# Optimization experiments

Hardware: AMD Instinct MI355X
Metric: run time of the kernel (lower is better)

The kernel has to match this reference:

```python
import jax, jax.numpy as jnp
import numpy as np

N = 50000      # nodes
E = 800000     # directed edges (before self-loops)
IN = 100       # ogbn-products feature dim
HID = 32       # hidden channels per head
H = 4          # heads
OUT = 47       # classes
NEG = 0.2      # GATConv default negative_slope


def setup_inputs() -> dict:
    key = jax.random.key(0)
    ks = jax.random.split(key, 24)
    def p(k, shape, fan_in):
        s = 1.0 / np.sqrt(fan_in)
        return jax.random.uniform(k, shape, dtype=jnp.float32, minval=-s, maxval=s)
    return {
        "x": jax.random.normal(ks[0], (N, IN), dtype=jnp.float32),
        "edge_index": jax.random.randint(ks[1], (2, E), 0, N, dtype=jnp.int64),
        # conv1: GATConv(IN, HID, heads=H, concat=True)
        "W1": p(ks[2], (H * HID, IN), IN),
        "att1_src": p(ks[3], (1, H, HID), HID),
        "att1_dst": p(ks[4], (1, H, HID), HID),
        "b1": jnp.zeros((H * HID,), jnp.float32),
        "Wl1": p(ks[5], (H * HID, IN), IN), "bl1": p(ks[6], (H * HID,), IN),
        # conv2: GATConv(H*HID, HID, heads=H, concat=True)
        "W2": p(ks[7], (H * HID, H * HID), H * HID),
        "att2_src": p(ks[8], (1, H, HID), HID),
        "att2_dst": p(ks[9], (1, H, HID), HID),
        "b2": jnp.zeros((H * HID,), jnp.float32),
        "Wl2": p(ks[10], (H * HID, H * HID), H * HID), "bl2": p(ks[11], (H * HID,), H * HID),
        # conv3: GATConv(H*HID, OUT, heads=H, concat=False)
        "W3": p(ks[12], (H * OUT, H * HID), H * HID),
        "att3_src": p(ks[13], (1, H, OUT), OUT),
        "att3_dst": p(ks[14], (1, H, OUT), OUT),
        "b3": jnp.zeros((OUT,), jnp.float32),
        "Wl3": p(ks[15], (OUT, H * HID), H * HID), "bl3": p(ks[16], (OUT,), H * HID),
    }


def gat_conv(x, src, dst, W, a_src, a_dst, b, concat):
    # x: [N, F_in]; src/dst: [E'] (self-loops included)
    h = (x @ W.T).reshape(N, H, -1)                 # [N, H, C]
    alpha_src = (h * a_src).sum(-1)                  # [N, H]
    alpha_dst = (h * a_dst).sum(-1)                  # [N, H]
    e = jax.nn.leaky_relu(alpha_src[src] + alpha_dst[dst], NEG)  # [E', H]
    # softmax over incoming edges of each destination node (stable)
    m = jax.ops.segment_max(e, dst, num_segments=N)              # [N, H]
    ex = jnp.exp(e - m[dst])
    denom = jax.ops.segment_sum(ex, dst, num_segments=N)         # [N, H]
    alpha = ex / (denom[dst] + 1e-16)                            # [E', H]
    out = jax.ops.segment_sum(alpha[:, :, None] * h[src], dst, num_segments=N)  # [N, H, C]
    out = out.reshape(N, -1) if concat else out.mean(axis=1)
    return out + b


def reference(x, edge_index, W1, att1_src, att1_dst, b1, Wl1, bl1,
              W2, att2_src, att2_dst, b2, Wl2, bl2,
              W3, att3_src, att3_dst, b3, Wl3, bl3):
    loop = jnp.arange(N, dtype=edge_index.dtype)
    src = jnp.concatenate([edge_index[0], loop])  # PyG GATConv add_self_loops=True
    dst = jnp.concatenate([edge_index[1], loop])
    h = jax.nn.relu(gat_conv(x, src, dst, W1, att1_src, att1_dst, b1, True) + x @ Wl1.T + bl1)
    # dropout p=0.3 is identity in eval mode
    h = jax.nn.relu(gat_conv(h, src, dst, W2, att2_src, att2_dst, b2, True) + h @ Wl2.T + bl2)
    h = gat_conv(h, src, dst, W3, att3_src, att3_dst, b3, False) + h @ Wl3.T + bl3
    return jax.nn.log_softmax(h, axis=-1)
```

## Files before the change

kernel.cpp:

```cpp
#include <hip/hip_runtime.h>
#include <hip/hip_bf16.h>
#include <math.h>

#define N_NODES 50000
#define N_EDGES 800000
#define E_TOT   (N_EDGES + N_NODES)
#define HEADS   4
#define NEG     0.2f
#define NROWT   3125
#define SCAN_NB 196
#define GGRID   782
#define EGRID   3321
#define CNT_NB  831

typedef __attribute__((ext_vector_type(8))) short short8;
typedef __attribute__((ext_vector_type(4))) float f32x4;

__device__ __forceinline__ float bf_lo(unsigned u) { return __uint_as_float(u << 16); }
__device__ __forceinline__ float bf_hi(unsigned u) { return __uint_as_float(u & 0xffff0000u); }
__device__ __forceinline__ unsigned short f2bbits(float f) {
    __hip_bfloat16 b = __float2bfloat16(f);
    return *reinterpret_cast<unsigned short*>(&b);
}
__device__ __forceinline__ float lrelu(float v) { return v > 0.f ? v : NEG * v; }

#define WALL_TOT 96256
#define PREP_TOT (WALL_TOT + N_NODES * 128 + 1024)
#define PREP_NB  ((PREP_TOT + 255) / 256)

__global__ void prep_count(const float* __restrict__ W1, const float* __restrict__ Wl1,
                           const float* __restrict__ W2, const float* __restrict__ Wl2,
                           const float* __restrict__ W3, const float* __restrict__ Wl3,
                           const float* __restrict__ a3s, const float* __restrict__ a3d,
                           const float* __restrict__ x,
                           unsigned short* __restrict__ WALL, unsigned short* __restrict__ Xb,
                           float* __restrict__ VS, float* __restrict__ VD,
                           const int* __restrict__ edst, int* __restrict__ cnt,
                           int* __restrict__ rank) {
    if (blockIdx.x < CNT_NB) {
        int base = blockIdx.x * 1024 + threadIdx.x;
        #pragma unroll
        for (int k = 0; k < 4; ++k) {
            int i = base + k * 256;
            if (i < E_TOT) {
                int d = (i < N_EDGES) ? edst[i] : (i - N_EDGES);
                rank[i] = atomicAdd(&cnt[d], 1);
            }
        }
        return;
    }
    int i = (blockIdx.x - CNT_NB) * 256 + threadIdx.x;
    if (i < WALL_TOT) {
        float v;
        if (i < 65536) {
            const float* src; int base, K;
            if      (i < 16384) { src = W1;  base = 0;     K = 100; }
            else if (i < 32768) { src = Wl1; base = 16384; K = 100; }
            else if (i < 49152) { src = W2;  base = 32768; K = 128; }
            else                { src = Wl2; base = 49152; K = 128; }
            int local = i - base;
            int m = local >> 7, k = local & 127;
            v = (k < K) ? src[m * K + k] : 0.f;
        } else if (i < 71680) {
            int local = i - 65536;
            int m = local >> 7, k = local & 127;
            v = (m < 47) ? Wl3[m * 128 + k] : 0.f;
        } else {
            int local = i - 71680;
            int c = local >> 9, k512 = local & 511;
            int h = k512 >> 7, kk = k512 & 127;
            v = (c < 47) ? 0.25f * W3[(h * 47 + c) * 128 + kk] : 0.f;
        }
        WALL[i] = f2bbits(v);
    } else if (i < WALL_TOT + N_NODES * 128) {
        int j = i - WALL_TOT;
        int n = j >> 7, k = j & 127;
        float v = (k < 100) ? x[n * 100 + k] : 0.f;
        Xb[j] = f2bbits(v);
    } else if (i < PREP_TOT) {
        int k = i - (WALL_TOT + N_NODES * 128);
        int sd = k >> 9, h = (k >> 7) & 3, kk = k & 127;
        const float* att = sd ? a3d : a3s;
        float s = 0.f;
        for (int c = 0; c < 47; ++c) s += att[h * 47 + c] * W3[(h * 47 + c) * 128 + kk];
        (sd ? VD : VS)[h * 128 + kk] = s;
    }
}


__global__ void scan_part1(const int* __restrict__ cnt, int* __restrict__ partial) {
    __shared__ int red[256];
    int t = threadIdx.x;
    int i = blockIdx.x * 256 + t;
    int v = (i < N_NODES) ? cnt[i] : 0;
    red[t] = v;
    __syncthreads();
    #pragma unroll
    for (int s = 128; s; s >>= 1) {
        if (t < s) red[t] += red[t + s];
        __syncthreads();
    }
    if (t == 0) partial[blockIdx.x] = red[0];
}

__global__ void scan_part2(int* __restrict__ partial) {
    __shared__ int sums[256];
    int t = threadIdx.x;
    int v = (t < SCAN_NB) ? partial[t] : 0;
    sums[t] = v;
    __syncthreads();
    #pragma unroll
    for (int d = 1; d < 256; d <<= 1) {
        int add = (t >= d) ? sums[t - d] : 0;
        __syncthreads();
        sums[t] += add;
        __syncthreads();
    }
    if (t < SCAN_NB) partial[t] = sums[t] - v;
}

__global__ void scan_part3(const int* __restrict__ cnt, const int* __restrict__ partial,
                           int* __restrict__ off) {
    __shared__ int sums[256];
    int t = threadIdx.x;
    int i = blockIdx.x * 256 + t;
    int v = (i < N_NODES) ? cnt[i] : 0;
    sums[t] = v;
    __syncthreads();
    #pragma unroll
    for (int d = 1; d < 256; d <<= 1) {
        int add = (t >= d) ? sums[t - d] : 0;
        __syncthreads();
        sums[t] += add;
        __syncthreads();
    }
    int excl = sums[t] - v + partial[blockIdx.x];
    if (i < N_NODES) off[i] = excl;
    if (i == N_NODES - 1) off[N_NODES] = excl + v;
}


__device__ __forceinline__ void gemm_dual_body(
        int rt,
        const unsigned short* __restrict__ A,
        const unsigned short* __restrict__ Wh, const unsigned short* __restrict__ Wl,
        const float* __restrict__ bl, const float* __restrict__ bagg,
        const float* __restrict__ att_s, const float* __restrict__ att_d,
        unsigned short* __restrict__ HFb, unsigned short* __restrict__ LINB,
        float* __restrict__ ASRC, float* __restrict__ ADST) {
    int lane = threadIdx.x & 63;
    if (rt >= NROWT) return;
    int l16 = lane & 15, kgrp = lane >> 4;
    const unsigned short* xrow = A + (size_t)(rt * 16 + l16) * 128 + kgrp * 8;
    short8 a[4];
    #pragma unroll
    for (int ks = 0; ks < 4; ++ks)
        a[ks] = *reinterpret_cast<const short8*>(xrow + ks * 32);
    int row0 = rt * 16 + kgrp * 4;
    float ps[4][4] = {}, pd[4][4] = {};
    #pragma unroll
    for (int ct = 0; ct < 16; ++ct) {
        const bool isH = (ct < 8);
        const unsigned short* W = isH ? Wh : Wl;
        int c = (isH ? ct : ct - 8) * 16 + l16;
        const unsigned short* wrow = W + (size_t)c * 128 + kgrp * 8;
        f32x4 acc = {0.f, 0.f, 0.f, 0.f};
        #pragma unroll
        for (int ks = 0; ks < 4; ++ks) {
            short8 b = *reinterpret_cast<const short8*>(wrow + ks * 32);
            acc = __builtin_amdgcn_mfma_f32_16x16x32_bf16(a[ks], b, acc, 0, 0, 0);
        }
        if (isH) {
            const int h = ct >> 1;
            float as = att_s[h * 32 + (ct & 1) * 16 + l16];
            float ad = att_d[h * 32 + (ct & 1) * 16 + l16];
            #pragma unroll
            for (int r = 0; r < 4; ++r) {
                ps[h][r] += acc[r] * as;
                pd[h][r] += acc[r] * ad;
                HFb[(size_t)(row0 + r) * 128 + c] = f2bbits(acc[r]);
            }
        } else {
            float bias = bl[c] + bagg[c];
            #pragma unroll
            for (int r = 0; r < 4; ++r)
                LINB[(size_t)(row0 + r) * 128 + c] = f2bbits(acc[r] + bias);
        }
    }
    #pragma unroll
    for (int h = 0; h < 4; ++h)
        #pragma unroll
        for (int r = 0; r < 4; ++r) {
            #pragma unroll
            for (int d = 1; d < 16; d <<= 1) {
                ps[h][r] += __shfl_xor(ps[h][r], d);
                pd[h][r] += __shfl_xor(pd[h][r], d);
            }
        }
    if (l16 == 0) {
        #pragma unroll
        for (int r = 0; r < 4; ++r)
            #pragma unroll
            for (int h = 0; h < 4; ++h) {
                ASRC[(row0 + r) * 4 + h] = ps[h][r];
                ADST[(row0 + r) * 4 + h] = pd[h][r];
            }
    }
}

__global__ __launch_bounds__(256) void gemm_dual_a(
        const unsigned short* __restrict__ A,
        const unsigned short* __restrict__ Wh, const unsigned short* __restrict__ Wl,
        const float* __restrict__ bl, const float* __restrict__ bagg,
        const float* __restrict__ att_s, const float* __restrict__ att_d,
        unsigned short* __restrict__ HFb, unsigned short* __restrict__ LINB,
        float* __restrict__ ASRC, float* __restrict__ ADST) {
    int rt = blockIdx.x * 4 + (threadIdx.x >> 6);
    gemm_dual_body(rt, A, Wh, Wl, bl, bagg, att_s, att_d, HFb, LINB, ASRC, ADST);
}

__global__ __launch_bounds__(256) void gemm1_scatter(
        const unsigned short* __restrict__ A,
        const unsigned short* __restrict__ Wh, const unsigned short* __restrict__ Wl,
        const float* __restrict__ bl, const float* __restrict__ bagg,
        const float* __restrict__ att_s, const float* __restrict__ att_d,
        unsigned short* __restrict__ HFb, unsigned short* __restrict__ LINB,
        float* __restrict__ ASRC, float* __restrict__ ADST,
        const int* __restrict__ esrc, const int* __restrict__ edst,
        const int* __restrict__ off, const int* __restrict__ rank,
        unsigned* __restrict__ csr) {
    if (blockIdx.x < GGRID) {
        int rt = blockIdx.x * 4 + (threadIdx.x >> 6);
        gemm_dual_body(rt, A, Wh, Wl, bl, bagg, att_s, att_d, HFb, LINB, ASRC, ADST);
        return;
    }
    int i = (blockIdx.x - GGRID) * 256 + threadIdx.x;
    if (i >= E_TOT) return;
    int s, d;
    if (i < N_EDGES) { s = esrc[i]; d = edst[i]; }
    else             { s = i - N_EDGES; d = s; }
    int pos = off[d] + rank[i];
    csr[pos] = ((unsigned)d << 16) | (unsigned)s;
}


__global__ void edge_weights(const unsigned* __restrict__ csr,
                             const float* __restrict__ asrc, const float* __restrict__ adst,
                             float4* __restrict__ W4) {
    int e = blockIdx.x * blockDim.x + threadIdx.x;
    if (e >= E_TOT) return;
    unsigned u = csr[e];
    int s = u & 0xffffu, d = u >> 16;
    float4 av = ((const float4*)asrc)[s];
    float4 dv = ((const float4*)adst)[d];
    float4 w;
    w.x = __expf(lrelu(av.x + dv.x));
    w.y = __expf(lrelu(av.y + dv.y));
    w.z = __expf(lrelu(av.z + dv.z));
    w.w = __expf(lrelu(av.w + dv.w));
    W4[e] = w;
}


template<bool ALPHA3>
__global__ __launch_bounds__(256) void agg12(
        const int* __restrict__ off, const unsigned* __restrict__ csr,
        const uint2* __restrict__ HU2,
        const float* __restrict__ asrc, const float* __restrict__ adst,
        const uint2* __restrict__ LINB2,
        unsigned* __restrict__ OUTB,
        const float4* __restrict__ VS4, const float4* __restrict__ VD4,
        float* __restrict__ ASRC3, float* __restrict__ ADST3) {
    int wv = threadIdx.x >> 6, lane = threadIdx.x & 63;
    int n = blockIdx.x * 4 + wv;
    int e0 = off[n], e1 = off[n + 1];
    int el = lane >> 5;
    int fl = lane & 31;
    int h = fl >> 3;
    float adh = adst[n * 4 + h];
    float acc0 = 0.f, acc1 = 0.f, acc2 = 0.f, acc3 = 0.f, den = 0.f;
    int e = e0;
    for (; e + 16 <= e1; e += 16) {
        int s[8]; float a[8]; uint2 u[8];
        #pragma unroll
        for (int j = 0; j < 8; ++j) s[j] = csr[e + 2 * j + el] & 0xffffu;
        #pragma unroll
        for (int j = 0; j < 8; ++j) a[j] = asrc[s[j] * 4 + h];
        #pragma unroll
        for (int j = 0; j < 8; ++j) u[j] = HU2[(size_t)s[j] * 32 + fl];
        #pragma unroll
        for (int j = 0; j < 8; ++j) {
            float w = __expf(lrelu(a[j] + adh));
            den += w;
            acc0 += w * bf_lo(u[j].x);
            acc1 += w * bf_hi(u[j].x);
            acc2 += w * bf_lo(u[j].y);
            acc3 += w * bf_hi(u[j].y);
        }
    }
    for (; e + 4 <= e1; e += 4) {
        int s[2]; float a[2]; uint2 u[2];
        #pragma unroll
        for (int j = 0; j < 2; ++j) s[j] = csr[e + 2 * j + el] & 0xffffu;
        #pragma unroll
        for (int j = 0; j < 2; ++j) a[j] = asrc[s[j] * 4 + h];
        #pragma unroll
        for (int j = 0; j < 2; ++j) u[j] = HU2[(size_t)s[j] * 32 + fl];
        #pragma unroll
        for (int j = 0; j < 2; ++j) {
            float w = __expf(lrelu(a[j] + adh));
            den += w;
            acc0 += w * bf_lo(u[j].x);
            acc1 += w * bf_hi(u[j].x);
            acc2 += w * bf_lo(u[j].y);
            acc3 += w * bf_hi(u[j].y);
        }
    }
    for (; e + 2 <= e1; e += 2) {
        int s = csr[e + el] & 0xffffu;
        float w = __expf(lrelu(asrc[s * 4 + h] + adh));
        uint2 u = HU2[(size_t)s * 32 + fl];
        den += w;
        acc0 += w * bf_lo(u.x);
        acc1 += w * bf_hi(u.x);
        acc2 += w * bf_lo(u.y);
        acc3 += w * bf_hi(u.y);
    }
    if (e + el < e1) {
        int s = csr[e + el] & 0xffffu;
        float w = __expf(lrelu(asrc[s * 4 + h] + adh));
        uint2 u = HU2[(size_t)s * 32 + fl];
        den += w;
        acc0 += w * bf_lo(u.x);
        acc1 += w * bf_hi(u.x);
        acc2 += w * bf_lo(u.y);
        acc3 += w * bf_hi(u.y);
    }
    acc0 += __shfl_xor(acc0, 32);
    acc1 += __shfl_xor(acc1, 32);
    acc2 += __shfl_xor(acc2, 32);
    acc3 += __shfl_xor(acc3, 32);
    den  += __shfl_xor(den, 32);
    float inv = 1.0f / (den + 1e-16f);
    uint2 lu = LINB2[(size_t)n * 32 + fl];
    float o0 = fmaxf(acc0 * inv + bf_lo(lu.x), 0.f);
    float o1 = fmaxf(acc1 * inv + bf_hi(lu.x), 0.f);
    float o2 = fmaxf(acc2 * inv + bf_lo(lu.y), 0.f);
    float o3 = fmaxf(acc3 * inv + bf_hi(lu.y), 0.f);
    if (el == 0) {
        uint2 p;
        p.x = ((unsigned)f2bbits(o1) << 16) | f2bbits(o0);
        p.y = ((unsigned)f2bbits(o3) << 16) | f2bbits(o2);
        ((uint2*)OUTB)[(size_t)n * 32 + fl] = p;
    }
    if (ALPHA3) {
        float ss[4], sd[4];
        #pragma unroll
        for (int hh = 0; hh < 4; ++hh) {
            float4 vs = VS4[hh * 32 + fl];
            float4 vd = VD4[hh * 32 + fl];
            ss[hh] = o0 * vs.x + o1 * vs.y + o2 * vs.z + o3 * vs.w;
            sd[hh] = o0 * vd.x + o1 * vd.y + o2 * vd.z + o3 * vd.w;
        }
        #pragma unroll
        for (int d2 = 1; d2 < 32; d2 <<= 1)
            #pragma unroll
            for (int hh = 0; hh < 4; ++hh) {
                ss[hh] += __shfl_xor(ss[hh], d2);
                sd[hh] += __shfl_xor(sd[hh], d2);
            }
        if (lane == 0) {
            #pragma unroll
            for (int hh = 0; hh < 4; ++hh) {
                ASRC3[n * 4 + hh] = ss[hh];
                ADST3[n * 4 + hh] = sd[hh];
            }
        }
    }
}


__global__ __launch_bounds__(256) void agg3f(
        const int* __restrict__ off, const unsigned* __restrict__ csr,
        const uint2* __restrict__ BU2,
        const float4* __restrict__ W4,
        uint2* __restrict__ AGG2) {
    int wv = threadIdx.x >> 6, lane = threadIdx.x & 63;
    int n = blockIdx.x * 4 + wv;
    int e0 = off[n], e1 = off[n + 1];
    int el = lane >> 5, fl = lane & 31;
    float acc[4][4] = {};
    float den[4] = {0.f, 0.f, 0.f, 0.f};
    int e = e0;
    for (; e + 16 <= e1; e += 16) {
        int s[8]; float4 w[8]; uint2 u[8];
        #pragma unroll
        for (int j = 0; j < 8; ++j) s[j] = csr[e + 2 * j + el] & 0xffffu;
        #pragma unroll
        for (int j = 0; j < 8; ++j) w[j] = W4[e + 2 * j + el];
        #pragma unroll
        for (int j = 0; j < 8; ++j) u[j] = BU2[(size_t)s[j] * 32 + fl];
        #pragma unroll
        for (int j = 0; j < 8; ++j) {
            float f0 = bf_lo(u[j].x), f1 = bf_hi(u[j].x);
            float f2 = bf_lo(u[j].y), f3 = bf_hi(u[j].y);
            den[0] += w[j].x; den[1] += w[j].y; den[2] += w[j].z; den[3] += w[j].w;
            acc[0][0] += w[j].x * f0; acc[0][1] += w[j].x * f1; acc[0][2] += w[j].x * f2; acc[0][3] += w[j].x * f3;
            acc[1][0] += w[j].y * f0; acc[1][1] += w[j].y * f1; acc[1][2] += w[j].y * f2; acc[1][3] += w[j].y * f3;
            acc[2][0] += w[j].z * f0; acc[2][1] += w[j].z * f1; acc[2][2] += w[j].z * f2; acc[2][3] += w[j].z * f3;
            acc[3][0] += w[j].w * f0; acc[3][1] += w[j].w * f1; acc[3][2] += w[j].w * f2; acc[3][3] += w[j].w * f3;
        }
    }
    for (; e + 2 <= e1; e += 2) {
        int s = csr[e + el] & 0xffffu;
        float4 w = W4[e + el];
        uint2 u = BU2[(size_t)s * 32 + fl];
        float f0 = bf_lo(u.x), f1 = bf_hi(u.x);
        float f2 = bf_lo(u.y), f3 = bf_hi(u.y);
        den[0] += w.x; den[1] += w.y; den[2] += w.z; den[3] += w.w;
        acc[0][0] += w.x * f0; acc[0][1] += w.x * f1; acc[0][2] += w.x * f2; acc[0][3] += w.x * f3;
        acc[1][0] += w.y * f0; acc[1][1] += w.y * f1; acc[1][2] += w.y * f2; acc[1][3] += w.y * f3;
        acc[2][0] += w.z * f0; acc[2][1] += w.z * f1; acc[2][2] += w.z * f2; acc[2][3] += w.z * f3;
        acc[3][0] += w.w * f0; acc[3][1] += w.w * f1; acc[3][2] += w.w * f2; acc[3][3] += w.w * f3;
    }
    if (e + el < e1) {
        int s = csr[e + el] & 0xffffu;
        float4 w = W4[e + el];
        uint2 u = BU2[(size_t)s * 32 + fl];
        float f0 = bf_lo(u.x), f1 = bf_hi(u.x);
        float f2 = bf_lo(u.y), f3 = bf_hi(u.y);
        den[0] += w.x; den[1] += w.y; den[2] += w.z; den[3] += w.w;
        acc[0][0] += w.x * f0; acc[0][1] += w.x * f1; acc[0][2] += w.x * f2; acc[0][3] += w.x * f3;
        acc[1][0] += w.y * f0; acc[1][1] += w.y * f1; acc[1][2] += w.y * f2; acc[1][3] += w.y * f3;
        acc[2][0] += w.z * f0; acc[2][1] += w.z * f1; acc[2][2] += w.z * f2; acc[2][3] += w.z * f3;
        acc[3][0] += w.w * f0; acc[3][1] += w.w * f1; acc[3][2] += w.w * f2; acc[3][3] += w.w * f3;
    }
    #pragma unroll
    for (int h = 0; h < 4; ++h) {
        den[h] += __shfl_xor(den[h], 32);
        #pragma unroll
        for (int k = 0; k < 4; ++k) acc[h][k] += __shfl_xor(acc[h][k], 32);
    }
    if (el == 0) {
        size_t base = (size_t)n * 128 + fl;
        #pragma unroll
        for (int h = 0; h < 4; ++h) {
            float inv = 1.0f / (den[h] + 1e-16f);
            uint2 p;
            p.x = ((unsigned)f2bbits(acc[h][1] * inv) << 16) | f2bbits(acc[h][0] * inv);
            p.y = ((unsigned)f2bbits(acc[h][3] * inv) << 16) | f2bbits(acc[h][2] * inv);
            AGG2[base + h * 32] = p;
        }
    }
}


__global__ __launch_bounds__(256) void post_ls(
        const unsigned short* __restrict__ AGG, const unsigned short* __restrict__ Bb,
        const unsigned short* __restrict__ W3m, const unsigned short* __restrict__ Wl3b,
        const float* __restrict__ b3, const float* __restrict__ bl3,
        float* __restrict__ OUT) {
    int wv = threadIdx.x >> 6, lane = threadIdx.x & 63;
    int rt = blockIdx.x * 4 + wv;
    if (rt >= NROWT) return;
    int l16 = lane & 15, kgrp = lane >> 4;
    const unsigned short* arow = AGG + (size_t)(rt * 16 + l16) * 512 + kgrp * 8;
    short8 a[16];
    #pragma unroll
    for (int ks = 0; ks < 16; ++ks)
        a[ks] = *reinterpret_cast<const short8*>(arow + ks * 32);
    const unsigned short* brow = Bb + (size_t)(rt * 16 + l16) * 128 + kgrp * 8;
    short8 al[4];
    #pragma unroll
    for (int ks = 0; ks < 4; ++ks)
        al[ks] = *reinterpret_cast<const short8*>(brow + ks * 32);
    f32x4 accs[3];
    #pragma unroll
    for (int ct = 0; ct < 3; ++ct) {
        int c = ct * 16 + l16;
        const unsigned short* wrow = W3m + (size_t)c * 512 + kgrp * 8;
        const unsigned short* lrow = Wl3b + (size_t)c * 128 + kgrp * 8;
        f32x4 acc = {0.f, 0.f, 0.f, 0.f};
        #pragma unroll
        for (int ks = 0; ks < 16; ++ks) {
            short8 b = *reinterpret_cast<const short8*>(wrow + ks * 32);
            acc = __builtin_amdgcn_mfma_f32_16x16x32_bf16(a[ks], b, acc, 0, 0, 0);
        }
        #pragma unroll
        for (int ks = 0; ks < 4; ++ks) {
            short8 b = *reinterpret_cast<const short8*>(lrow + ks * 32);
            acc = __builtin_amdgcn_mfma_f32_16x16x32_bf16(al[ks], b, acc, 0, 0, 0);
        }
        accs[ct] = acc;
    }
    int row0 = rt * 16 + kgrp * 4;
    int c0 = l16, c1 = 16 + l16, c2 = 32 + l16;
    bool v2 = (c2 < 47);
    float b0 = b3[c0] + bl3[c0];
    float b1v = b3[c1] + bl3[c1];
    float b2v = v2 ? (b3[c2] + bl3[c2]) : 0.f;
    #pragma unroll
    for (int r = 0; r < 4; ++r) {
        int row = row0 + r;
        float z0 = accs[0][r] + b0;
        float z1 = accs[1][r] + b1v;
        float z2 = v2 ? (accs[2][r] + b2v) : -INFINITY;
        float m = fmaxf(fmaxf(z0, z1), z2);
        #pragma unroll
        for (int d = 1; d < 16; d <<= 1) m = fmaxf(m, __shfl_xor(m, d));
        float s = __expf(z0 - m) + __expf(z1 - m) + (v2 ? __expf(z2 - m) : 0.f);
        #pragma unroll
        for (int d = 1; d < 16; d <<= 1) s += __shfl_xor(s, d);
        float ls = logf(s);
        float* orow = OUT + (size_t)row * 47;
        orow[c0] = z0 - m - ls;
        orow[c1] = z1 - m - ls;
        if (v2) orow[c2] = z2 - m - ls;
    }
}


extern "C" void kernel_launch(void* const* d_in, const int* in_sizes, int n_in,
                              void* d_out, int out_size, void* d_ws, size_t ws_size,
                              hipStream_t stream) {
    const float* x   = (const float*)d_in[0];
    const int*   ei  = (const int*)d_in[1];
    const float* W1  = (const float*)d_in[2];
    const float* a1s = (const float*)d_in[3];
    const float* a1d = (const float*)d_in[4];
    const float* b1  = (const float*)d_in[5];
    const float* Wl1 = (const float*)d_in[6];
    const float* bl1 = (const float*)d_in[7];
    const float* W2  = (const float*)d_in[8];
    const float* a2s = (const float*)d_in[9];
    const float* a2d = (const float*)d_in[10];
    const float* b2  = (const float*)d_in[11];
    const float* Wl2 = (const float*)d_in[12];
    const float* bl2 = (const float*)d_in[13];
    const float* W3  = (const float*)d_in[14];
    const float* a3s = (const float*)d_in[15];
    const float* a3d = (const float*)d_in[16];
    const float* b3  = (const float*)d_in[17];
    const float* Wl3 = (const float*)d_in[18];
    const float* bl3 = (const float*)d_in[19];
    float* out = (float*)d_out;

    size_t cur = 0;
    char* wsb = (char*)d_ws;
    auto carve = [&](size_t bytes) -> void* {
        void* p = wsb + cur;
        cur += (bytes + 255) & ~(size_t)255;
        return p;
    };
    int*   cnt    = (int*)  carve((size_t)N_NODES * 4);
    int*   offs   = (int*)  carve((size_t)(N_NODES + 1) * 4);
    int*   part   = (int*)  carve((size_t)SCAN_NB * 4);
    int*   rank   = (int*)  carve((size_t)E_TOT * 4);
    unsigned* csr = (unsigned*)carve((size_t)E_TOT * 4);
    unsigned short* WALL = (unsigned short*)carve((size_t)WALL_TOT * 2);
    unsigned short* Xb   = (unsigned short*)carve((size_t)N_NODES * 128 * 2);
    unsigned short* HFb  = (unsigned short*)carve((size_t)N_NODES * 128 * 2);
    unsigned short* LINB = (unsigned short*)carve((size_t)N_NODES * 128 * 2);
    carve((size_t)N_NODES * 128 * 2);
    unsigned short* AGG  = Xb;
    unsigned short* Bb   = (unsigned short*)carve((size_t)N_NODES * 128 * 2);
    float* ASRC   = (float*)carve((size_t)N_NODES * 4 * 4);
    float* ADST   = (float*)carve((size_t)N_NODES * 4 * 4);
    float* ASRC3  = (float*)carve((size_t)N_NODES * 4 * 4);
    float* ADST3  = (float*)carve((size_t)N_NODES * 4 * 4);
    float4* W4    = (float4*)carve((size_t)E_TOT * 16);
    float* VS     = (float*)carve((size_t)4 * 128 * 4);
    float* VD     = (float*)carve((size_t)4 * 128 * 4);

    unsigned short* Wb1h = WALL + 0;
    unsigned short* Wb1l = WALL + 16384;
    unsigned short* Wb2h = WALL + 32768;
    unsigned short* Wb2l = WALL + 49152;
    unsigned short* Wb3l = WALL + 65536;
    unsigned short* W3m  = WALL + 71680;

    const int* esrc = ei;
    const int* edst = ei + N_EDGES;

    hipMemsetAsync(cnt, 0, (size_t)N_NODES * 4, stream);
    prep_count<<<CNT_NB + PREP_NB, 256, 0, stream>>>(W1, Wl1, W2, Wl2, W3, Wl3, a3s, a3d,
                                                     x, WALL, Xb, VS, VD, edst, cnt, rank);
    scan_part1<<<SCAN_NB, 256, 0, stream>>>(cnt, part);
    scan_part2<<<1, 256, 0, stream>>>(part);
    scan_part3<<<SCAN_NB, 256, 0, stream>>>(cnt, part, offs);

    int ngrid = N_NODES / 4;

    gemm1_scatter<<<GGRID + EGRID, 256, 0, stream>>>(Xb, Wb1h, Wb1l, bl1, b1, a1s, a1d,
                                                     HFb, LINB, ASRC, ADST,
                                                     esrc, edst, offs, rank, csr);
    agg12<false><<<ngrid, 256, 0, stream>>>(offs, csr, (const uint2*)HFb, ASRC, ADST,
                                            (const uint2*)LINB, (unsigned*)Bb,
                                            nullptr, nullptr, nullptr, nullptr);
    gemm_dual_a<<<GGRID, 256, 0, stream>>>(Bb, Wb2h, Wb2l, bl2, b2, a2s, a2d,
                                           HFb, LINB, ASRC, ADST);
    agg12<true><<<ngrid, 256, 0, stream>>>(offs, csr, (const uint2*)HFb, ASRC, ADST,
                                           (const uint2*)LINB, (unsigned*)Bb,
                                           (const float4*)VS, (const float4*)VD,
                                           ASRC3, ADST3);
    edge_weights<<<EGRID, 256, 0, stream>>>(csr, ASRC3, ADST3, W4);
    agg3f<<<ngrid, 256, 0, stream>>>(offs, csr, (const uint2*)Bb, W4, (uint2*)AGG);
    post_ls<<<GGRID, 256, 0, stream>>>(AGG, Bb, W3m, Wb3l, b3, bl3, out);
}
```

Before: 323.1 us.

## Fuse layer-3 aggregation with output GEMM and log-softmax via shared memory

Result: no change. 325.5 us (+0.7%).

```diff
diff --git a/kernel.cpp b/kernel.cpp
--- a/kernel.cpp
+++ b/kernel.cpp
@@ -380,13 +380,20 @@
 }
 
 
-__global__ __launch_bounds__(256) void agg3f(
+#define AGGP 520
+
+__global__ __launch_bounds__(1024) void agg3_post(
         const int* __restrict__ off, const unsigned* __restrict__ csr,
         const uint2* __restrict__ BU2,
         const float4* __restrict__ W4,
-        uint2* __restrict__ AGG2) {
+        const unsigned short* __restrict__ Bb,
+        const unsigned short* __restrict__ W3m, const unsigned short* __restrict__ Wl3b,
+        const float* __restrict__ b3, const float* __restrict__ bl3,
+        float* __restrict__ OUT) {
+    __shared__ unsigned short AGGs[16][AGGP];
     int wv = threadIdx.x >> 6, lane = threadIdx.x & 63;
-    int n = blockIdx.x * 4 + wv;
+    int n0 = blockIdx.x * 16;
+    int n = n0 + wv;
     int e0 = off[n], e1 = off[n + 1];
     int el = lane >> 5, fl = lane & 31;
     float acc[4][4] = {};
@@ -442,58 +449,44 @@
         for (int k = 0; k < 4; ++k) acc[h][k] += __shfl_xor(acc[h][k], 32);
     }
     if (el == 0) {
-        size_t base = (size_t)n * 128 + fl;
+        unsigned short* row = &AGGs[wv][0];
         #pragma unroll
         for (int h = 0; h < 4; ++h) {
             float inv = 1.0f / (den[h] + 1e-16f);
-            uint2 p;
-            p.x = ((unsigned)f2bbits(acc[h][1] * inv) << 16) | f2bbits(acc[h][0] * inv);
-            p.y = ((unsigned)f2bbits(acc[h][3] * inv) << 16) | f2bbits(acc[h][2] * inv);
-            AGG2[base + h * 32] = p;
-        }
-    }
-}
-
-
-__global__ __launch_bounds__(256) void post_ls(
-        const unsigned short* __restrict__ AGG, const unsigned short* __restrict__ Bb,
-        const unsigned short* __restrict__ W3m, const unsigned short* __restrict__ Wl3b,
-        const float* __restrict__ b3, const float* __restrict__ bl3,
-        float* __restrict__ OUT) {
-    int wv = threadIdx.x >> 6, lane = threadIdx.x & 63;
-    int rt = blockIdx.x * 4 + wv;
-    if (rt >= NROWT) return;
+            int f = h * 128 + 4 * fl;
+            row[f]     = f2bbits(acc[h][0] * inv);
+            row[f + 1] = f2bbits(acc[h][1] * inv);
+            row[f + 2] = f2bbits(acc[h][2] * inv);
+            row[f + 3] = f2bbits(acc[h][3] * inv);
+        }
+    }
+    __syncthreads();
+    if (wv != 0) return;
     int l16 = lane & 15, kgrp = lane >> 4;
-    const unsigned short* arow = AGG + (size_t)(rt * 16 + l16) * 512 + kgrp * 8;
-    short8 a[16];
-    #pragma unroll
-    for (int ks = 0; ks < 16; ++ks)
-        a[ks] = *reinterpret_cast<const short8*>(arow + ks * 32);
-    const unsigned short* brow = Bb + (size_t)(rt * 16 + l16) * 128 + kgrp * 8;
-    short8 al[4];
-    #pragma unroll
-    for (int ks = 0; ks < 4; ++ks)
-        al[ks] = *reinterpret_cast<const short8*>(brow + ks * 32);
+    const unsigned short* arow = &AGGs[l16][kgrp * 8];
+    const unsigned short* brow = Bb + (size_t)(n0 + l16) * 128 + kgrp * 8;
     f32x4 accs[3];
     #pragma unroll
     for (int ct = 0; ct < 3; ++ct) {
         int c = ct * 16 + l16;
         const unsigned short* wrow = W3m + (size_t)c * 512 + kgrp * 8;
         const unsigned short* lrow = Wl3b + (size_t)c * 128 + kgrp * 8;
-        f32x4 acc = {0.f, 0.f, 0.f, 0.f};
+        f32x4 acc2 = {0.f, 0.f, 0.f, 0.f};
         #pragma unroll
         for (int ks = 0; ks < 16; ++ks) {
+            short8 av = *reinterpret_cast<const short8*>(arow + ks * 32);
             short8 b = *reinterpret_cast<const short8*>(wrow + ks * 32);
-            acc = __builtin_amdgcn_mfma_f32_16x16x32_bf16(a[ks], b, acc, 0, 0, 0);
+            acc2 = __builtin_amdgcn_mfma_f32_16x16x32_bf16(av, b, acc2, 0, 0, 0);
         }
         #pragma unroll
         for (int ks = 0; ks < 4; ++ks) {
+            short8 av = *reinterpret_cast<const short8*>(brow + ks * 32);
             short8 b = *reinterpret_cast<const short8*>(lrow + ks * 32);
-            acc = __builtin_amdgcn_mfma_f32_16x16x32_bf16(al[ks], b, acc, 0, 0, 0);
-        }
-        accs[ct] = acc;
-    }
-    int row0 = rt * 16 + kgrp * 4;
+            acc2 = __builtin_amdgcn_mfma_f32_16x16x32_bf16(av, b, acc2, 0, 0, 0);
+        }
+        accs[ct] = acc2;
+    }
+    int row0 = n0 + kgrp * 4;
     int c0 = l16, c1 = 16 + l16, c2 = 32 + l16;
     bool v2 = (c2 < 47);
     float b0 = b3[c0] + bl3[c0];
@@ -561,8 +554,6 @@
     unsigned short* Xb   = (unsigned short*)carve((size_t)N_NODES * 128 * 2);
     unsigned short* HFb  = (unsigned short*)carve((size_t)N_NODES * 128 * 2);
     unsigned short* LINB = (unsigned short*)carve((size_t)N_NODES * 128 * 2);
-    carve((size_t)N_NODES * 128 * 2);
-    unsigned short* AGG  = Xb;
     unsigned short* Bb   = (unsigned short*)carve((size_t)N_NODES * 128 * 2);
     float* ASRC   = (float*)carve((size_t)N_NODES * 4 * 4);
     float* ADST   = (float*)carve((size_t)N_NODES * 4 * 4);
@@ -604,6 +595,6 @@
                                            (const float4*)VS, (const float4*)VD,
                                            ASRC3, ADST3);
     edge_weights<<<EGRID, 256, 0, stream>>>(csr, ASRC3, ADST3, W4);
-    agg3f<<<ngrid, 256, 0, stream>>>(offs, csr, (const uint2*)Bb, W4, (uint2*)AGG);
-    post_ls<<<GGRID, 256, 0, stream>>>(AGG, Bb, W3m, Wb3l, b3, bl3, out);
-}
+    agg3_post<<<NROWT, 1024, 0, stream>>>(offs, csr, (const uint2*)Bb, W4,
+                                          Bb, W3m, Wb3l, b3, bl3, out);
+}
```
